# Kernel optimization log

Hardware: AMD Instinct MI355X
Metric: run time of the kernel (lower is better)

## Reference

```python
import jax, jax.numpy as jnp
import numpy as np

N_NODES = 50000
N_EDGES = 1600000


def setup_inputs() -> dict:
    key = jax.random.key(0)
    ks = jax.random.split(key, 8)
    dims = [1024, 2048, 1024, 512]
    fea = jax.random.normal(ks[0], (N_NODES, dims[0]), dtype=jnp.float32)
    edge_index = jax.random.randint(ks[1], (2, N_EDGES), 0, N_NODES, dtype=jnp.int64)
    edge_vals = jax.random.uniform(ks[2], (N_EDGES,), dtype=jnp.float32)
    # Glorot-ish scaled weights per GCN layer
    W1 = jax.random.normal(ks[3], (dims[0], dims[1]), dtype=jnp.float32) / np.sqrt(dims[0])
    W2 = jax.random.normal(ks[4], (dims[1], dims[2]), dtype=jnp.float32) / np.sqrt(dims[1])
    W3 = jax.random.normal(ks[5], (dims[2], dims[3]), dtype=jnp.float32) / np.sqrt(dims[2])
    b1 = jnp.zeros((dims[1],), dtype=jnp.float32)
    b2 = jnp.zeros((dims[2],), dtype=jnp.float32)
    b3 = jnp.zeros((dims[3],), dtype=jnp.float32)
    return {"fea": fea, "edge_index": edge_index, "edge_vals": edge_vals,
            "W1": W1, "b1": b1, "W2": W2, "b2": b2, "W3": W3, "b3": b3}


def _gcn_layer(x, row, col, edge_vals, W, b):
    # dense transform: [N, din] @ [din, dout] + bias
    support = x @ W + b
    # spmm(adj, support) in COO form: out[row] += val * support[col]
    msgs = support[col] * edge_vals[:, None]          # [E, dout]
    return jax.ops.segment_sum(msgs, row, num_segments=N_NODES)


def reference(fea, edge_index, edge_vals, W1, b1, W2, b2, W3, b3):
    row, col = edge_index[0], edge_index[1]
    h = jax.nn.relu(_gcn_layer(fea, row, col, edge_vals, W1, b1))
    h = jax.nn.relu(_gcn_layer(h, row, col, edge_vals, W2, b2))
    # last layer: no activation
    return _gcn_layer(h, row, col, edge_vals, W3, b3)
```

## Files before the change

### kernel.cpp

```cpp
#include <hip/hip_runtime.h>

typedef unsigned short u16;
using bf16x8 = __attribute__((ext_vector_type(8))) short;
using u16x8  = __attribute__((ext_vector_type(8))) unsigned short;
using u16x4  = __attribute__((ext_vector_type(4))) unsigned short;
using f32x4  = __attribute__((ext_vector_type(4))) float;

#define NN 50000
#define NPAD 50176

__device__ __forceinline__ u16 f2b(float f) {
  union { float f; unsigned u; } x; x.f = f;
  unsigned r = x.u + 0x7fffu + ((x.u >> 16) & 1u);
  return (u16)(r >> 16);
}
__device__ __forceinline__ float b2f(u16 h) {
  union { unsigned u; float f; } x; x.u = ((unsigned)h) << 16; return x.f;
}

#define GLOAD_LDS16(g, l) __builtin_amdgcn_global_load_lds( \
    (const __attribute__((address_space(1))) unsigned int*)(g), \
    (__attribute__((address_space(3))) unsigned int*)(l), 16, 0, 0)

__global__ void hist_kernel(const int* __restrict__ rows, const float* __restrict__ vals,
                            int* __restrict__ counts, float* __restrict__ rowsum, int E) {
  int e = blockIdx.x * 256 + threadIdx.x;
  if (e < E) {
    int r = rows[e];
    atomicAdd(&counts[r], 1);
    atomicAdd(&rowsum[r], vals[e]);
  }
}

__global__ void scan_bsum(const int* __restrict__ counts, int* __restrict__ bsum, int n) {
  __shared__ int s[256];
  int t = threadIdx.x;
  int gi = blockIdx.x * 256 + t;
  s[t] = (gi < n) ? counts[gi] : 0;
  __syncthreads();
  for (int d = 128; d > 0; d >>= 1) {
    if (t < d) s[t] += s[t + d];
    __syncthreads();
  }
  if (t == 0) bsum[blockIdx.x] = s[0];
}

__global__ void scan_partials(int* __restrict__ bsum, int nb) {
  __shared__ int s[256];
  int t = threadIdx.x;
  int v = (t < nb) ? bsum[t] : 0;
  s[t] = v;
  __syncthreads();
  for (int d = 1; d < 256; d <<= 1) {
    int x = (t >= d) ? s[t - d] : 0;
    __syncthreads();
    s[t] += x;
    __syncthreads();
  }
  if (t < nb) bsum[t] = s[t] - v;
}

__global__ void scan_final(const int* __restrict__ counts, const int* __restrict__ bsum,
                           int* __restrict__ offs, int n) {
  __shared__ int s[256];
  int t = threadIdx.x;
  int gi = blockIdx.x * 256 + t;
  int v = (gi < n) ? counts[gi] : 0;
  s[t] = v;
  __syncthreads();
  for (int d = 1; d < 256; d <<= 1) {
    int x = (t >= d) ? s[t - d] : 0;
    __syncthreads();
    s[t] += x;
    __syncthreads();
  }
  if (gi <= n) offs[gi] = bsum[blockIdx.x] + s[t] - v;
}

__global__ void scatter_kernel(const int* __restrict__ rows, const int* __restrict__ cols,
                               const float* __restrict__ vals, const int* __restrict__ offs,
                               int* __restrict__ cursor, int* __restrict__ ecol,
                               float* __restrict__ ev2, int E) {
  int e = blockIdx.x * 256 + threadIdx.x;
  if (e < E) {
    int r = rows[e];
    int p = offs[r] + atomicAdd(&cursor[r], 1);
    ecol[p] = cols[e];
    ev2[p] = vals[e];
  }
}

__global__ void conv_f2b4(const float* __restrict__ in, u16* __restrict__ out, int n4) {
  int i = blockIdx.x * 256 + threadIdx.x;
  if (i < n4) {
    float4 f = ((const float4*)in)[i];
    ushort4 o;
    o.x = f2b(f.x); o.y = f2b(f.y); o.z = f2b(f.z); o.w = f2b(f.w);
    ((ushort4*)out)[i] = o;
  }
}

__global__ void transpose_conv(const float* __restrict__ W, u16* __restrict__ Wt, int K, int N) {
  __shared__ float tile[32][33];
  int bx = blockIdx.x * 32;
  int by = blockIdx.y * 32;
  int tx = threadIdx.x;
  int ty = threadIdx.y;
  for (int i = 0; i < 32; i += 8) tile[ty + i][tx] = W[(size_t)(by + ty + i) * N + bx + tx];
  __syncthreads();
  for (int i = 0; i < 32; i += 8) Wt[(size_t)(bx + ty + i) * K + by + tx] = f2b(tile[tx][ty + i]);
}

__global__ __launch_bounds__(512, 4)
void gemm256(const u16* __restrict__ A, const u16* __restrict__ Bt,
             const float* __restrict__ bias, const float* __restrict__ rowsum,
             u16* __restrict__ C, int M, int N, int K, int relu, int nbx) {
  __shared__ __align__(16) u16 lds[3][12288];

  const int p = blockIdx.x, total = gridDim.x;
  const int q = total >> 3, r8 = total & 7;
  const int xcd = p & 7, slot_ = p >> 3;
  const int l = (xcd < r8 ? xcd * (q + 1) : r8 * (q + 1) + (xcd - r8) * q) + slot_;
  const int bm = (l / nbx) * 256;
  const int bn = (l % nbx) * 128;

  const int tid = threadIdx.x;
  const int lane = tid & 63;
  const int wid = tid >> 6;
  const int wm = wid >> 1;
  const int wn = wid & 1;
  const int l15 = lane & 15, lg = lane >> 4;

  const int trow = tid >> 2;
  const int xcol = (tid & 3) ^ ((tid >> 3) & 3);
  const u16* gA = A + (size_t)(bm + trow) * K + xcol * 8;
  const u16* gB = Bt + (size_t)(bn + trow) * K + xcol * 8;
  const size_t rowstep = (size_t)128 * K;

  f32x4 acc[4][4];
#pragma unroll
  for (int i = 0; i < 4; i++)
#pragma unroll
    for (int j = 0; j < 4; j++)
#pragma unroll
      for (int k = 0; k < 4; k++) acc[i][j][k] = 0.f;

  const int NT = K >> 5;

#define STAGE(kt, b)                                                           \
  {                                                                            \
    const u16* sa = gA + (size_t)(kt) * 32;                                    \
    u16* da = &lds[b][0] + tid * 8;                                            \
    GLOAD_LDS16(sa, da);                                                       \
    GLOAD_LDS16(sa + rowstep, da + 4096);                                      \
    const u16* sb = gB + (size_t)(kt) * 32;                                    \
    GLOAD_LDS16(sb, &lds[b][8192] + tid * 8);                                  \
  }

  STAGE(0, 0);
  STAGE(1, 1);

  for (int u = 0; u < NT; u++) {
    const int cb = u % 3;
    if (u + 2 < NT) {
      STAGE(u + 2, (u + 2) % 3);
      asm volatile("s_waitcnt vmcnt(6)" ::: "memory");
    } else if (u + 1 < NT) {
      asm volatile("s_waitcnt vmcnt(3)" ::: "memory");
    } else {
      asm volatile("s_waitcnt vmcnt(0)" ::: "memory");
    }
    __builtin_amdgcn_s_barrier();

    const u16* ab = &lds[cb][0];
    const u16* bb = &lds[cb][8192];

    bf16x8 bfr[4];
#pragma unroll
    for (int n = 0; n < 4; n++) {
      int row = wn * 64 + n * 16 + l15;
      int s = lg ^ ((row >> 1) & 3);
      bfr[n] = *(const bf16x8*)&bb[row * 32 + s * 8];
    }
    __builtin_amdgcn_s_setprio(1);
#pragma unroll
    for (int m = 0; m < 4; m++) {
      int row = wm * 64 + m * 16 + l15;
      int s = lg ^ ((row >> 1) & 3);
      bf16x8 am = *(const bf16x8*)&ab[row * 32 + s * 8];
#pragma unroll
      for (int n = 0; n < 4; n++)
        acc[m][n] = __builtin_amdgcn_mfma_f32_16x16x32_bf16(am, bfr[n], acc[m][n], 0, 0, 0);
    }
    __builtin_amdgcn_s_setprio(0);
    asm volatile("s_waitcnt lgkmcnt(0)" ::: "memory");
    __builtin_amdgcn_s_barrier();
  }
#undef STAGE

  u16* eb = &lds[0][0] + wid * 4096;
  float bs[4];
#pragma unroll
  for (int n = 0; n < 4; n++) bs[n] = bias[bn + wn * 64 + n * 16 + l15];
#pragma unroll
  for (int m = 0; m < 4; m++) {
    int r0 = m * 16 + lg * 4;
#pragma unroll
    for (int j = 0; j < 4; j++) {
      int r = r0 + j;
      float rs = rowsum ? rowsum[bm + wm * 64 + r] : 1.0f;
#pragma unroll
      for (int n = 0; n < 4; n++) {
        int c = n * 16 + l15;
        float v = acc[m][n][j] + rs * bs[n];
        if (relu) v = fmaxf(v, 0.f);
        int cs = (c & 7) | ((((c >> 3) ^ (r & 7)) & 7) << 3);
        eb[r * 64 + cs] = f2b(v);
      }
    }
  }
  asm volatile("s_waitcnt lgkmcnt(0)" ::: "memory");
#pragma unroll
  for (int pass = 0; pass < 8; pass++) {
    int r = pass * 8 + (lane >> 3);
    int ch = lane & 7;
    int chs = ch ^ (r & 7);
    u16x8 val = *(const u16x8*)&eb[r * 64 + chs * 8];
    int grow = bm + wm * 64 + r;
    if (grow < M)
      *(u16x8*)&C[(size_t)grow * N + bn + wn * 64 + ch * 8] = val;
  }
}

template <int VEC, int RELU, int OUTF32>
__global__ __launch_bounds__(64)
void spmm3(const int* __restrict__ offs, const int* __restrict__ ecol,
           const float* __restrict__ ev, const u16* __restrict__ X,
           void* __restrict__ outp, int stride) {
  const int node = blockIdx.x;
  const int t = threadIdx.x;
  const int s0 = offs[node];
  const int e0 = offs[node + 1];
  float acc[VEC];
#pragma unroll
  for (int k = 0; k < VEC; k++) acc[k] = 0.f;
  const u16* __restrict__ Xc = X + (size_t)t * VEC;

  int j = s0;
  for (; j + 4 <= e0; j += 4) {
    const int c0 = ecol[j], c1 = ecol[j + 1], c2 = ecol[j + 2], c3 = ecol[j + 3];
    const float v0 = ev[j], v1 = ev[j + 1], v2 = ev[j + 2], v3 = ev[j + 3];
    u16 a0[VEC], a1[VEC], a2[VEC], a3[VEC];
    if constexpr (VEC == 8) {
      *(u16x8*)a0 = *(const u16x8*)(Xc + (size_t)c0 * stride);
      *(u16x8*)a1 = *(const u16x8*)(Xc + (size_t)c1 * stride);
      *(u16x8*)a2 = *(const u16x8*)(Xc + (size_t)c2 * stride);
      *(u16x8*)a3 = *(const u16x8*)(Xc + (size_t)c3 * stride);
    } else {
      *(u16x4*)a0 = *(const u16x4*)(Xc + (size_t)c0 * stride);
      *(u16x4*)a1 = *(const u16x4*)(Xc + (size_t)c1 * stride);
      *(u16x4*)a2 = *(const u16x4*)(Xc + (size_t)c2 * stride);
      *(u16x4*)a3 = *(const u16x4*)(Xc + (size_t)c3 * stride);
    }
#pragma unroll
    for (int k = 0; k < VEC; k++) acc[k] += v0 * b2f(a0[k]);
#pragma unroll
    for (int k = 0; k < VEC; k++) acc[k] += v1 * b2f(a1[k]);
#pragma unroll
    for (int k = 0; k < VEC; k++) acc[k] += v2 * b2f(a2[k]);
#pragma unroll
    for (int k = 0; k < VEC; k++) acc[k] += v3 * b2f(a3[k]);
  }
  for (; j < e0; j++) {
    const int c0 = ecol[j];
    const float v0 = ev[j];
    u16 a0[VEC];
    if constexpr (VEC == 8) {
      *(u16x8*)a0 = *(const u16x8*)(Xc + (size_t)c0 * stride);
    } else {
      *(u16x4*)a0 = *(const u16x4*)(Xc + (size_t)c0 * stride);
    }
#pragma unroll
    for (int k = 0; k < VEC; k++) acc[k] += v0 * b2f(a0[k]);
  }

  if (RELU) {
#pragma unroll
    for (int k = 0; k < VEC; k++) acc[k] = fmaxf(acc[k], 0.f);
  }
  if (OUTF32) {
    float* o = (float*)outp + (size_t)node * stride + (size_t)t * VEC;
#pragma unroll
    for (int k = 0; k < VEC; k += 4) {
      f32x4 st;
      st[0] = acc[k]; st[1] = acc[k + 1]; st[2] = acc[k + 2]; st[3] = acc[k + 3];
      __builtin_nontemporal_store(st, (f32x4*)(o + k));
    }
  } else {
    u16* o = (u16*)outp + (size_t)node * stride + (size_t)t * VEC;
    if constexpr (VEC == 8) {
      u16x8 st;
#pragma unroll
      for (int k = 0; k < 8; k++) st[k] = f2b(acc[k]);
      __builtin_nontemporal_store(st, (u16x8*)o);
    } else {
      u16x4 st;
      st[0] = f2b(acc[0]); st[1] = f2b(acc[1]); st[2] = f2b(acc[2]); st[3] = f2b(acc[3]);
      __builtin_nontemporal_store(st, (u16x4*)o);
    }
  }
}

extern "C" void kernel_launch(void* const* d_in, const int* in_sizes, int n_in,
                              void* d_out, int out_size, void* d_ws, size_t ws_size,
                              hipStream_t stream) {
  const float* fea = (const float*)d_in[0];
  const int* ei = (const int*)d_in[1];
  const float* ev = (const float*)d_in[2];
  const float* W1 = (const float*)d_in[3];
  const float* b1 = (const float*)d_in[4];
  const float* W2 = (const float*)d_in[5];
  const float* b2 = (const float*)d_in[6];
  const float* W3 = (const float*)d_in[7];
  const float* b3 = (const float*)d_in[8];
  const int E = in_sizes[1] / 2;
  const int* erow = ei;
  const int* ecol_in = ei + E;

  char* w = (char*)d_ws;
  auto alloc = [&](size_t bytes) {
    char* p = w;
    w += (bytes + 255) & ~(size_t)255;
    return p;
  };
  u16* fea_b = (u16*)alloc((size_t)NPAD * 1024 * 2);
  u16* bufB  = (u16*)alloc((size_t)NPAD * 1024 * 2);
  u16* h1_b  = (u16*)alloc((size_t)NPAD * 2048 * 2);
  u16* t2_b  = (u16*)alloc((size_t)NPAD * 1024 * 2);
  u16* W1t = (u16*)alloc((size_t)2048 * 1024 * 2);
  u16* W2t = (u16*)alloc((size_t)1024 * 2048 * 2);
  u16* W3t = (u16*)alloc((size_t)512 * 1024 * 2);
  float* rowsum = (float*)alloc((size_t)NN * 4);
  int* counts = (int*)alloc((size_t)NN * 4);
  int* cursor = (int*)alloc((size_t)NN * 4);
  int* offs = (int*)alloc((size_t)(NN + 1) * 4);
  int* ecol = (int*)alloc((size_t)E * 4);
  float* ev2 = (float*)alloc((size_t)E * 4);
  int* bsum = (int*)alloc(256 * 4);
  (void)bsum; (void)ws_size; (void)n_in; (void)out_size;

  hipMemsetAsync(rowsum, 0, (size_t)((char*)offs - (char*)rowsum), stream);

  const int eb = (E + 255) / 256;
  const int nb = (NN + 256) / 256;
  hist_kernel<<<eb, 256, 0, stream>>>(erow, ev, counts, rowsum, E);
  scan_bsum<<<nb, 256, 0, stream>>>(counts, bsum, NN);
  scan_partials<<<1, 256, 0, stream>>>(bsum, nb);
  scan_final<<<nb, 256, 0, stream>>>(counts, bsum, offs, NN);
  scatter_kernel<<<eb, 256, 0, stream>>>(erow, ecol_in, ev, offs, cursor, ecol, ev2, E);

  conv_f2b4<<<(NN * 1024 / 4 + 255) / 256, 256, 0, stream>>>(fea, fea_b, NN * 1024 / 4);
  dim3 tb(32, 8);
  transpose_conv<<<dim3(2048 / 32, 1024 / 32), tb, 0, stream>>>(W1, W1t, 1024, 2048);
  transpose_conv<<<dim3(1024 / 32, 2048 / 32), tb, 0, stream>>>(W2, W2t, 2048, 1024);
  transpose_conv<<<dim3(512 / 32, 1024 / 32), tb, 0, stream>>>(W3, W3t, 1024, 512);

  const int MT2 = (NN + 255) / 256;
  spmm3<8, 0, 0><<<NN, 64, 0, stream>>>(offs, ecol, ev2, fea_b, bufB, 1024);
  spmm3<8, 0, 0><<<NN, 64, 0, stream>>>(offs, ecol, ev2, fea_b + 512, bufB + 512, 1024);
  gemm256<<<(2048 / 128) * MT2, 512, 0, stream>>>(bufB, W1t, b1, rowsum, h1_b, NN, 2048, 1024, 1, 2048 / 128);
  gemm256<<<(1024 / 128) * MT2, 512, 0, stream>>>(h1_b, W2t, b2, nullptr, t2_b, NN, 1024, 2048, 0, 1024 / 128);
  spmm3<8, 1, 0><<<NN, 64, 0, stream>>>(offs, ecol, ev2, t2_b, fea_b, 1024);
  spmm3<8, 1, 0><<<NN, 64, 0, stream>>>(offs, ecol, ev2, t2_b + 512, fea_b + 512, 1024);
  gemm256<<<(512 / 128) * MT2, 512, 0, stream>>>(fea_b, W3t, b3, nullptr, bufB, NN, 512, 1024, 0, 512 / 128);
  spmm3<4, 0, 1><<<NN, 64, 0, stream>>>(offs, ecol, ev2, bufB, d_out, 512);
  spmm3<4, 0, 1><<<NN, 64, 0, stream>>>(offs, ecol, ev2, bufB + 256, (float*)d_out + 256, 512);
}
```

Measured before the change: 1.995 ms.

## Process two K-tiles per barrier pair with 4-buffer LDS ring in GEMM

The bf16 MFMA GEMM main loop now stages two K-tiles at a time into a four-deep LDS ring and runs two tiles of MFMAs between each barrier pair. This halves the number of barriers and waitcnt points per K step. The epilogue is reworked to stage one 16-row slab per wave at a time through a smaller LDS region, and the launch bound hint is raised. The larger LDS footprint, about 96 KB per block, likely allows only one 512-thread block per CU, so fewer waves are available to hide latency. The loop also assumes an even number of K-tiles.

```diff
diff --git a/kernel.cpp b/kernel.cpp
--- a/kernel.cpp
+++ b/kernel.cpp
@@ -111,11 +111,11 @@
   for (int i = 0; i < 32; i += 8) Wt[(size_t)(bx + ty + i) * K + by + tx] = f2b(tile[tx][ty + i]);
 }
 
-__global__ __launch_bounds__(512, 4)
+__global__ __launch_bounds__(512, 6)
 void gemm256(const u16* __restrict__ A, const u16* __restrict__ Bt,
              const float* __restrict__ bias, const float* __restrict__ rowsum,
              u16* __restrict__ C, int M, int N, int K, int relu, int nbx) {
-  __shared__ __align__(16) u16 lds[3][12288];
+  __shared__ __align__(16) u16 lds[4][12288];
 
   const int p = blockIdx.x, total = gridDim.x;
   const int q = total >> 3, r8 = total & 7;
@@ -157,78 +157,82 @@
     GLOAD_LDS16(sb, &lds[b][8192] + tid * 8);                                  \
   }
 
+#define TILE_MFMA(buf)                                                         \
+  {                                                                            \
+    const u16* ab = &lds[buf][0];                                              \
+    const u16* bb = &lds[buf][8192];                                           \
+    bf16x8 bfr[4];                                                             \
+    _Pragma("unroll") for (int n = 0; n < 4; n++) {                            \
+      int row = wn * 64 + n * 16 + l15;                                        \
+      int s = lg ^ ((row >> 1) & 3);                                           \
+      bfr[n] = *(const bf16x8*)&bb[row * 32 + s * 8];                          \
+    }                                                                          \
+    __builtin_amdgcn_s_setprio(1);                                             \
+    _Pragma("unroll") for (int m = 0; m < 4; m++) {                            \
+      int row = wm * 64 + m * 16 + l15;                                        \
+      int s = lg ^ ((row >> 1) & 3);                                           \
+      bf16x8 am = *(const bf16x8*)&ab[row * 32 + s * 8];                       \
+      _Pragma("unroll") for (int n = 0; n < 4; n++)                            \
+        acc[m][n] = __builtin_amdgcn_mfma_f32_16x16x32_bf16(am, bfr[n],        \
+                                                            acc[m][n], 0, 0, 0); \
+    }                                                                          \
+    __builtin_amdgcn_s_setprio(0);                                             \
+  }
+
   STAGE(0, 0);
   STAGE(1, 1);
 
-  for (int u = 0; u < NT; u++) {
-    const int cb = u % 3;
+  for (int u = 0; u < NT; u += 2) {
     if (u + 2 < NT) {
-      STAGE(u + 2, (u + 2) % 3);
+      STAGE(u + 2, (u + 2) & 3);
+      STAGE(u + 3, (u + 3) & 3);
       asm volatile("s_waitcnt vmcnt(6)" ::: "memory");
-    } else if (u + 1 < NT) {
-      asm volatile("s_waitcnt vmcnt(3)" ::: "memory");
     } else {
       asm volatile("s_waitcnt vmcnt(0)" ::: "memory");
     }
     __builtin_amdgcn_s_barrier();
 
-    const u16* ab = &lds[cb][0];
-    const u16* bb = &lds[cb][8192];
-
-    bf16x8 bfr[4];
-#pragma unroll
-    for (int n = 0; n < 4; n++) {
-      int row = wn * 64 + n * 16 + l15;
-      int s = lg ^ ((row >> 1) & 3);
-      bfr[n] = *(const bf16x8*)&bb[row * 32 + s * 8];
-    }
-    __builtin_amdgcn_s_setprio(1);
-#pragma unroll
-    for (int m = 0; m < 4; m++) {
-      int row = wm * 64 + m * 16 + l15;
-      int s = lg ^ ((row >> 1) & 3);
-      bf16x8 am = *(const bf16x8*)&ab[row * 32 + s * 8];
-#pragma unroll
-      for (int n = 0; n < 4; n++)
-        acc[m][n] = __builtin_amdgcn_mfma_f32_16x16x32_bf16(am, bfr[n], acc[m][n], 0, 0, 0);
-    }
-    __builtin_amdgcn_s_setprio(0);
+    TILE_MFMA(u & 3);
+    TILE_MFMA((u + 1) & 3);
+
     asm volatile("s_waitcnt lgkmcnt(0)" ::: "memory");
     __builtin_amdgcn_s_barrier();
   }
 #undef STAGE
-
-  u16* eb = &lds[0][0] + wid * 4096;
+#undef TILE_MFMA
+
+  u16* eb = &lds[0][0] + wid * 1024;
   float bs[4];
 #pragma unroll
   for (int n = 0; n < 4; n++) bs[n] = bias[bn + wn * 64 + n * 16 + l15];
 #pragma unroll
   for (int m = 0; m < 4; m++) {
-    int r0 = m * 16 + lg * 4;
 #pragma unroll
     for (int j = 0; j < 4; j++) {
-      int r = r0 + j;
-      float rs = rowsum ? rowsum[bm + wm * 64 + r] : 1.0f;
+      int rr = lg * 4 + j;
+      float rs = rowsum ? rowsum[bm + wm * 64 + m * 16 + rr] : 1.0f;
 #pragma unroll
       for (int n = 0; n < 4; n++) {
         int c = n * 16 + l15;
         float v = acc[m][n][j] + rs * bs[n];
         if (relu) v = fmaxf(v, 0.f);
-        int cs = (c & 7) | ((((c >> 3) ^ (r & 7)) & 7) << 3);
-        eb[r * 64 + cs] = f2b(v);
+        int cs = (c & 7) | ((((c >> 3) ^ (rr & 7)) & 7) << 3);
+        eb[rr * 64 + cs] = f2b(v);
       }
     }
-  }
-  asm volatile("s_waitcnt lgkmcnt(0)" ::: "memory");
-#pragma unroll
-  for (int pass = 0; pass < 8; pass++) {
-    int r = pass * 8 + (lane >> 3);
-    int ch = lane & 7;
-    int chs = ch ^ (r & 7);
-    u16x8 val = *(const u16x8*)&eb[r * 64 + chs * 8];
-    int grow = bm + wm * 64 + r;
-    if (grow < M)
-      *(u16x8*)&C[(size_t)grow * N + bn + wn * 64 + ch * 8] = val;
+    asm volatile("s_waitcnt lgkmcnt(0)" ::: "memory");
+#pragma unroll
+    for (int pass = 0; pass < 2; pass++) {
+      int idx = pass * 64 + lane;
+      int rr = idx >> 3;
+      int ch = idx & 7;
+      int chs = ch ^ (rr & 7);
+      u16x8 val = *(const u16x8*)&eb[rr * 64 + chs * 8];
+      int grow = bm + wm * 64 + m * 16 + rr;
+      if (grow < M)
+        *(u16x8*)&C[(size_t)grow * N + bn + wn * 64 + ch * 8] = val;
+    }
+    asm volatile("s_waitcnt lgkmcnt(0)" ::: "memory");
   }
 }
 
```

Result: slower. 2.284 ms (+14.5%).
